# Kernel optimization log

Measured on AMD Instinct MI355X. Metric: run time of the kernel, lower is better.

The kernel has to match this reference:

```python
import jax, jax.numpy as jnp
import numpy as np

IN_C = 256
N_E = 8192
E_DIM = 256
BETA = 0.25
K = 3
LN_EPS = 1e-5


def _conv(x, w, b):
    # x: [B,C,H,W], w: [O,I,K,K]
    y = jax.lax.conv_general_dilated(
        x, w, window_strides=(1, 1), padding='SAME',
        dimension_numbers=('NCHW', 'OIHW', 'NCHW'))
    return y + b[None, :, None, None]


def _layernorm(x, g, b):
    mu = jnp.mean(x, axis=-1, keepdims=True)
    var = jnp.var(x, axis=-1, keepdims=True)
    return (x - mu) * jax.lax.rsqrt(var + LN_EPS) * g + b


def setup_inputs() -> dict:
    key = jax.random.key(0)
    ks = jax.random.split(key, 8)
    fan_emb = IN_C * K * K
    fan_unemb = E_DIM * K * K
    return {
        'z': jax.random.normal(ks[0], (16, IN_C, 32, 32), dtype=jnp.float32),
        'emb_w': jax.random.normal(ks[1], (E_DIM, IN_C, K, K), dtype=jnp.float32) / np.sqrt(fan_emb),
        'emb_b': jnp.zeros((E_DIM,), dtype=jnp.float32),
        'ln_g': jnp.ones((E_DIM,), dtype=jnp.float32),
        'ln_b': jnp.zeros((E_DIM,), dtype=jnp.float32),
        'codebook': jax.random.uniform(ks[2], (N_E, E_DIM), dtype=jnp.float32,
                                       minval=-1.0 / N_E, maxval=1.0 / N_E),
        'unemb_w': jax.random.normal(ks[3], (IN_C, E_DIM, K, K), dtype=jnp.float32) / np.sqrt(fan_unemb),
        'unemb_b': jnp.zeros((IN_C,), dtype=jnp.float32),
    }


def reference(z, emb_w, emb_b, ln_g, ln_b, codebook, unemb_w, unemb_b):
    B, _, H, W = z.shape
    # emb conv, then b c h w -> b h w c
    ze = _conv(z, emb_w, emb_b)                       # [B,E,H,W]
    ze = jnp.transpose(ze, (0, 2, 3, 1))              # [B,H,W,E]
    zf = _layernorm(ze.reshape(B, H * W, E_DIM), ln_g, ln_b)
    zf = zf.reshape(-1, E_DIM)                        # [B*H*W, E]
    # squared distances: ||z||^2 + ||e||^2 - 2 z e^T
    d = (jnp.sum(zf ** 2, axis=1, keepdims=True)
         + jnp.sum(codebook ** 2, axis=1)[None, :]
         - 2.0 * jnp.einsum('bd,nd->bn', zf, codebook))  # [B*H*W, N_E]
    idx = jnp.argmin(d, axis=1)                       # [B*H*W]
    z_q = codebook[idx].reshape(ze.shape)             # [B,H,W,E]
    # legacy loss
    loss = (jnp.mean((jax.lax.stop_gradient(z_q) - ze) ** 2)
            + BETA * jnp.mean((z_q - jax.lax.stop_gradient(ze)) ** 2))
    # straight-through
    z_q = ze + jax.lax.stop_gradient(z_q - ze)
    z_q = jnp.transpose(z_q, (0, 3, 1, 2))            # [B,E,H,W]
    out = _conv(z_q, unemb_w, unemb_b)                # [B,C,H,W]
    return out, loss, idx
```

## Files before the change

kernel.cpp:

```cpp
#include <hip/hip_runtime.h>
#include <hip/hip_bf16.h>

#define B_SZ 16
#define CIN 256
#define EDIM 256
#define NE 8192
#define HW 32
#define NPIX (B_SZ*HW*HW)
#define OUT_ELEMS (B_SZ*CIN*HW*HW)
#define SCREEN_T 3.2e-4f
#define CAND_H 64

typedef __attribute__((ext_vector_type(8))) short short8;
typedef __attribute__((ext_vector_type(4))) short short4v;
typedef __attribute__((ext_vector_type(4))) float f32x4;

__device__ __forceinline__ float block_sum(float v, float* sbuf) {
    #pragma unroll
    for (int off = 32; off > 0; off >>= 1) v += __shfl_down(v, off, 64);
    int wid = threadIdx.x >> 6;
    int lane = threadIdx.x & 63;
    if (lane == 0) sbuf[wid] = v;
    __syncthreads();
    if (threadIdx.x == 0) sbuf[0] = sbuf[0] + sbuf[1] + sbuf[2] + sbuf[3];
    __syncthreads();
    float r = sbuf[0];
    __syncthreads();
    return r;
}

__device__ __forceinline__ double wave_sum_d(double v) {
    #pragma unroll
    for (int off = 32; off > 0; off >>= 1) v += __shfl_down(v, off, 64);
    return __shfl(v, 0, 64);
}

__device__ __forceinline__ unsigned short bf16rne(float f) {
    unsigned int u = __float_as_uint(f);
    unsigned int r = (u + 0x7FFFu + ((u >> 16) & 1u)) >> 16;
    return (unsigned short)r;
}
__device__ __forceinline__ float bf2f(unsigned short h) {
    return __uint_as_float((unsigned int)h << 16);
}

__device__ __forceinline__ unsigned int mapU(float f) {
    unsigned int u = __float_as_uint(f);
    return (u & 0x80000000u) ? ~u : (u | 0x80000000u);
}
__device__ __forceinline__ float unmapU(unsigned int m) {
    unsigned int u = (m & 0x80000000u) ? (m ^ 0x80000000u) : ~m;
    return __uint_as_float(u);
}

__global__ void prep_kernel(const float* __restrict__ emb_w, unsigned short* __restrict__ w1bh,
                            unsigned short* __restrict__ w1bl,
                            const float* __restrict__ unemb_w, unsigned short* __restrict__ w2hi,
                            unsigned short* __restrict__ w2lo, const float* __restrict__ cb,
                            unsigned short* __restrict__ cbhi, unsigned short* __restrict__ cblo) {
    int blk = blockIdx.x;
    if (blk < 2304) {
        int e = blk / 9, tap = blk % 9;
        int c = threadIdx.x;
        float v = emb_w[(size_t)e * 2304 + c * 9 + tap];
        unsigned short h = bf16rne(v);
        unsigned short l = bf16rne(v - bf2f(h));
        size_t j = (size_t)e * 2304 + tap * 256 + c;
        w1bh[j] = h; w1bl[j] = l;
    } else if (blk < 4608) {
        int b2 = blk - 2304;
        int cout = b2 / 9, tap = b2 % 9;
        int e = threadIdx.x;
        float v = unemb_w[(size_t)cout * 2304 + e * 9 + tap];
        unsigned short h = bf16rne(v);
        unsigned short l = bf16rne(v - bf2f(h));
        size_t j = (size_t)cout * 2304 + tap * 256 + e;
        w2hi[j] = h; w2lo[j] = l;
    } else {
        int i = (blk - 4608) * 256 + threadIdx.x;
        size_t base = (size_t)i * 4;
        float4 v = *(const float4*)(cb + base);
        short4v sh, sl;
        unsigned short h;
        h = bf16rne(v.x); sh[0] = (short)h; sl[0] = (short)bf16rne(v.x - bf2f(h));
        h = bf16rne(v.y); sh[1] = (short)h; sl[1] = (short)bf16rne(v.y - bf2f(h));
        h = bf16rne(v.z); sh[2] = (short)h; sl[2] = (short)bf16rne(v.z - bf2f(h));
        h = bf16rne(v.w); sh[3] = (short)h; sl[3] = (short)bf16rne(v.w - bf2f(h));
        *(short4v*)(cbhi + base) = sh;
        *(short4v*)(cblo + base) = sl;
    }
}

#define EM_REG 6528
__global__ __launch_bounds__(256, 4) void conv_emb_mfma(const float* __restrict__ z,
                                                        const unsigned short* __restrict__ w1bh,
                                                        const unsigned short* __restrict__ w1bl,
                                                        float* __restrict__ ze) {
    __shared__ char smem[3 * EM_REG];
    const int tid = threadIdx.x;
    const int wid = tid >> 6, lane = tid & 63;
    const int l15 = lane & 15, lg = lane >> 4;
    const int bh = blockIdx.x;
    const int b = bh >> 5, h = bh & 31;
    const int ch = blockIdx.y;

    for (int i = tid; i < (3 * EM_REG) / 16; i += 256) ((int4*)smem)[i] = make_int4(0, 0, 0, 0);

    const f32x4 zero4 = {0.f, 0.f, 0.f, 0.f};
    f32x4 acc[2][2];
    acc[0][0] = zero4; acc[0][1] = zero4; acc[1][0] = zero4; acc[1][1] = zero4;

    for (int cc = 0; cc < 256; cc += 32) {
        __syncthreads();
        #pragma unroll
        for (int rd = 0; rd < 2; ++rd) {
            int t2 = rd * 256 + tid;
            if (t2 < 408) {
                int row = t2 >> 2;
                int oct = t2 & 3;
                int r = row / 34, wp = row - r * 34;
                int hh = h + r - 1;
                if (hh >= 0 && hh < 32 && wp >= 1 && wp <= 32) {
                    const float* zp = z + (size_t)b * 262144 + (size_t)(cc + oct * 8) * 1024
                                    + hh * 32 + (wp - 1);
                    short8 vh, vm, vl;
                    #pragma unroll
                    for (int j = 0; j < 8; ++j) {
                        float v = zp[(size_t)j * 1024];
                        unsigned short h1 = bf16rne(v);
                        float rm = v - bf2f(h1);
                        unsigned short m1 = bf16rne(rm);
                        float rl = rm - bf2f(m1);
                        unsigned short l1 = bf16rne(rl);
                        vh[j] = (short)h1; vm[j] = (short)m1; vl[j] = (short)l1;
                    }
                    int boff = row * 64 + ((oct * 16) ^ ((wp & 3) << 4));
                    *(short8*)(smem + boff) = vh;
                    *(short8*)(smem + EM_REG + boff) = vm;
                    *(short8*)(smem + 2 * EM_REG + boff) = vl;
                }
            }
        }
        __syncthreads();

        #pragma unroll
        for (int tap = 0; tap < 9; ++tap) {
            const int r = tap / 3, kw = tap % 3;
            short8 a1[2], a2[2], a3[2], bhf[2], blf[2];
            #pragma unroll
            for (int mf = 0; mf < 2; ++mf) {
                int wpr = mf * 16 + l15 + kw;
                int boff = (r * 34 + wpr) * 64 + ((lg * 16) ^ ((wpr & 3) << 4));
                a1[mf] = *(const short8*)(smem + boff);
                a2[mf] = *(const short8*)(smem + EM_REG + boff);
                a3[mf] = *(const short8*)(smem + 2 * EM_REG + boff);
            }
            #pragma unroll
            for (int nf = 0; nf < 2; ++nf) {
                int e_idx = (ch << 7) + (wid << 5) + (nf << 4) + l15;
                size_t goff = (size_t)e_idx * 2304 + tap * 256 + cc + lg * 8;
                bhf[nf] = *(const short8*)(w1bh + goff);
                blf[nf] = *(const short8*)(w1bl + goff);
            }
            #pragma unroll
            for (int mf = 0; mf < 2; ++mf)
                #pragma unroll
                for (int nf = 0; nf < 2; ++nf) {
                    acc[mf][nf] = __builtin_amdgcn_mfma_f32_16x16x32_bf16(a1[mf], bhf[nf], acc[mf][nf], 0, 0, 0);
                    acc[mf][nf] = __builtin_amdgcn_mfma_f32_16x16x32_bf16(a1[mf], blf[nf], acc[mf][nf], 0, 0, 0);
                    acc[mf][nf] = __builtin_amdgcn_mfma_f32_16x16x32_bf16(a2[mf], bhf[nf], acc[mf][nf], 0, 0, 0);
                    acc[mf][nf] = __builtin_amdgcn_mfma_f32_16x16x32_bf16(a2[mf], blf[nf], acc[mf][nf], 0, 0, 0);
                    acc[mf][nf] = __builtin_amdgcn_mfma_f32_16x16x32_bf16(a3[mf], bhf[nf], acc[mf][nf], 0, 0, 0);
                }
        }
    }

    int p0 = (b * 32 + h) * 32;
    #pragma unroll
    for (int mf = 0; mf < 2; ++mf)
        #pragma unroll
        for (int nf = 0; nf < 2; ++nf) {
            int e_idx = (ch << 7) + (wid << 5) + (nf << 4) + l15;
            #pragma unroll
            for (int rr = 0; rr < 4; ++rr) {
                int pix = mf * 16 + lg * 4 + rr;
                ze[(size_t)(p0 + pix) * 256 + e_idx] = acc[mf][nf][rr];
            }
        }
}

__global__ __launch_bounds__(256) void ln_kernel(float* __restrict__ ze, const float* __restrict__ bias,
                                                 const float* __restrict__ g,
                                                 const float* __restrict__ bta,
                                                 unsigned short* __restrict__ zfb,
                                                 float* __restrict__ snorm, float* __restrict__ mu_a,
                                                 float* __restrict__ r_a) {
    int wid = threadIdx.x >> 6, lane = threadIdx.x & 63;
    int p = blockIdx.x * 4 + wid;
    float* zp = ze + (size_t)p * 256;
    float x0 = zp[lane]       + bias[lane];
    float x1 = zp[lane + 64]  + bias[lane + 64];
    float x2 = zp[lane + 128] + bias[lane + 128];
    float x3 = zp[lane + 192] + bias[lane + 192];
    zp[lane] = x0; zp[lane + 64] = x1; zp[lane + 128] = x2; zp[lane + 192] = x3;
    double lsum = (((double)x0 + (double)x1) + (double)x2) + (double)x3;
    double sum = wave_sum_d(lsum);
    float mu = ((float)sum) / 256.0f;
    float e0 = x0 - mu, e1 = x1 - mu, e2 = x2 - mu, e3 = x3 - mu;
    double lsq = (((double)(e0 * e0) + (double)(e1 * e1)) + (double)(e2 * e2)) + (double)(e3 * e3);
    double vs = wave_sum_d(lsq);
    float var = ((float)vs) / 256.0f;
    float r = 1.0f / sqrtf(var + 1e-5f);
    float y0 = ((e0 * r) * g[lane])       + bta[lane];
    float y1 = ((e1 * r) * g[lane + 64])  + bta[lane + 64];
    float y2 = ((e2 * r) * g[lane + 128]) + bta[lane + 128];
    float y3 = ((e3 * r) * g[lane + 192]) + bta[lane + 192];
    unsigned short* zq = zfb + (size_t)p * 256;
    zq[lane] = bf16rne(y0); zq[lane + 64] = bf16rne(y1);
    zq[lane + 128] = bf16rne(y2); zq[lane + 192] = bf16rne(y3);
    double lys = (((double)(y0 * y0) + (double)(y1 * y1)) + (double)(y2 * y2)) + (double)(y3 * y3);
    double ss = wave_sum_d(lys);
    if (lane == 0) { snorm[p] = (float)ss; mu_a[p] = mu; r_a[p] = r; }
}

__global__ __launch_bounds__(512) void screen_kernel(const unsigned short* __restrict__ zf_bf,
                                                     const unsigned short* __restrict__ cb_bf,
                                                     int* __restrict__ ccnt,
                                                     int* __restrict__ cand) {
    __shared__ unsigned int smax[64];
    __shared__ int scnt[64];
    __shared__ int sbuf[64][CAND_H];
    const int tid = threadIdx.x;
    const int w = tid >> 6;
    const int lane = tid & 63;
    const int l15 = lane & 15, lg = lane >> 4;
    const int p0 = blockIdx.x * 64;
    const int nh = blockIdx.y;
    const int nbase = nh << 12;
    const int rowoff = w * 16 + l15;
    const int lg8 = lg * 8;

    if (tid < 64) { smax[tid] = 0u; scnt[tid] = 0; }
    __syncthreads();

    short8 aF[4][8];
    #pragma unroll
    for (int mf = 0; mf < 4; ++mf)
        #pragma unroll
        for (int ks = 0; ks < 8; ++ks)
            aF[mf][ks] = *reinterpret_cast<const short8*>(
                zf_bf + (size_t)(p0 + mf * 16 + l15) * 256 + ks * 32 + lg8);

    const f32x4 zero4 = {0.f, 0.f, 0.f, 0.f};
    float runL[4][4], runS[4][4];
    #pragma unroll
    for (int mf = 0; mf < 4; ++mf)
        #pragma unroll
        for (int r = 0; r < 4; ++r) { runL[mf][r] = -3.4e38f; runS[mf][r] = -3.4e38f; }

    const unsigned short* basep = cb_bf + (size_t)(nbase + rowoff) * 256 + lg8;

    for (int c = 0; c < 4; ++c) {
        const unsigned short* bp = basep + (size_t)c * 128 * 256;
        short8 bF[8];
        #pragma unroll
        for (int ks = 0; ks < 8; ++ks) bF[ks] = *reinterpret_cast<const short8*>(bp + ks * 32);
        f32x4 acc[4] = {zero4, zero4, zero4, zero4};
        #pragma unroll
        for (int ks = 0; ks < 8; ++ks)
            #pragma unroll
            for (int mf = 0; mf < 4; ++mf)
                acc[mf] = __builtin_amdgcn_mfma_f32_16x16x32_bf16(aF[mf][ks], bF[ks], acc[mf], 0, 0, 0);
        #pragma unroll
        for (int mf = 0; mf < 4; ++mf)
            #pragma unroll
            for (int r = 0; r < 4; ++r) runL[mf][r] = fmaxf(runL[mf][r], acc[mf][r]);
    }
    #pragma unroll
    for (int mf = 0; mf < 4; ++mf)
        #pragma unroll
        for (int r = 0; r < 4; ++r) {
            float v = runL[mf][r];
            v = fmaxf(v, __shfl_xor(v, 1, 64));
            v = fmaxf(v, __shfl_xor(v, 2, 64));
            v = fmaxf(v, __shfl_xor(v, 4, 64));
            v = fmaxf(v, __shfl_xor(v, 8, 64));
            runL[mf][r] = v;
            if (l15 == 0) atomicMax(&smax[mf * 16 + lg * 4 + r], mapU(v));
        }
    __syncthreads();
    #pragma unroll
    for (int mf = 0; mf < 4; ++mf)
        #pragma unroll
        for (int r = 0; r < 4; ++r) runS[mf][r] = unmapU(smax[mf * 16 + lg * 4 + r]);

    for (int c = 0; c < 32; ++c) {
        const int nrow = nbase + c * 128 + rowoff;
        const unsigned short* bp = basep + (size_t)c * 128 * 256;
        short8 bF[8];
        #pragma unroll
        for (int ks = 0; ks < 8; ++ks) bF[ks] = *reinterpret_cast<const short8*>(bp + ks * 32);
        f32x4 acc[4] = {zero4, zero4, zero4, zero4};
        #pragma unroll
        for (int ks = 0; ks < 8; ++ks)
            #pragma unroll
            for (int mf = 0; mf < 4; ++mf)
                acc[mf] = __builtin_amdgcn_mfma_f32_16x16x32_bf16(aF[mf][ks], bF[ks], acc[mf], 0, 0, 0);

        unsigned qual = 0u;
        #pragma unroll
        for (int mf = 0; mf < 4; ++mf)
            #pragma unroll
            for (int r = 0; r < 4; ++r) {
                float dd = acc[mf][r];
                if (dd >= fmaxf(runS[mf][r], runL[mf][r]) - SCREEN_T) qual |= (1u << (mf * 4 + r));
                runL[mf][r] = fmaxf(runL[mf][r], dd);
            }
        if (qual) {
            #pragma unroll
            for (int mf = 0; mf < 4; ++mf)
                #pragma unroll
                for (int r = 0; r < 4; ++r)
                    if (qual & (1u << (mf * 4 + r))) {
                        int pix = mf * 16 + lg * 4 + r;
                        int s = atomicAdd(&scnt[pix], 1);
                        if (s < CAND_H) sbuf[pix][s] = nrow;
                    }
        }
        if ((c & 7) == 7) {
            #pragma unroll
            for (int mf = 0; mf < 4; ++mf)
                #pragma unroll
                for (int r = 0; r < 4; ++r) {
                    float v = runL[mf][r];
                    v = fmaxf(v, __shfl_xor(v, 1, 64));
                    v = fmaxf(v, __shfl_xor(v, 2, 64));
                    v = fmaxf(v, __shfl_xor(v, 4, 64));
                    v = fmaxf(v, __shfl_xor(v, 8, 64));
                    runL[mf][r] = v;
                    if (l15 == 0) atomicMax(&smax[mf * 16 + lg * 4 + r], mapU(v));
                }
            #pragma unroll
            for (int mf = 0; mf < 4; ++mf)
                #pragma unroll
                for (int r = 0; r < 4; ++r) runS[mf][r] = unmapU(smax[mf * 16 + lg * 4 + r]);
        }
    }
    __syncthreads();
    if (tid < 64) {
        int v = scnt[tid];
        ccnt[nh * NPIX + p0 + tid] = (v < CAND_H) ? v : CAND_H;
    }
    for (int i = tid; i < 64 * CAND_H; i += 512) {
        int pix = i >> 6;
        int s = i & (CAND_H - 1);
        if (s < scnt[pix])
            cand[(size_t)(p0 + pix) * 128 + nh * CAND_H + s] = sbuf[pix][s];
    }
}

__global__ __launch_bounds__(256) void rescore_kernel(const float* __restrict__ ze,
                                                      const float* __restrict__ mu_a,
                                                      const float* __restrict__ r_a,
                                                      const float* __restrict__ snorm,
                                                      const float* __restrict__ g,
                                                      const float* __restrict__ bta,
                                                      const float* __restrict__ cb,
                                                      const int* __restrict__ ccnt,
                                                      const int* __restrict__ cand,
                                                      int* __restrict__ idx_i,
                                                      float* __restrict__ idx_f) {
    int p = blockIdx.x * 4 + (threadIdx.x >> 6);
    int lane = threadIdx.x & 63;
    int cnt0 = ccnt[p];           if (cnt0 > CAND_H) cnt0 = CAND_H;
    int cnt1 = ccnt[NPIX + p];    if (cnt1 > CAND_H) cnt1 = CAND_H;
    int total = cnt0 + cnt1;
    float d = 3.4e38f;
    int ix = 0x7FFFFFFF;
    float mu = mu_a[p];
    float r = r_a[p];
    float sz = snorm[p];
    const float* zr = ze + (size_t)p * 256;
    for (int s = lane; s < total; s += 64) {
        int n = (s < cnt0) ? cand[(size_t)p * 128 + s]
                           : cand[(size_t)p * 128 + CAND_H + (s - cnt0)];
        const float* cr = cb + (size_t)n * 256;
        float a0 = 0.f, a1 = 0.f, a2 = 0.f, a3 = 0.f;
        for (int k0 = 0; k0 < 256; k0 += 4) {
            float4 zq = *(const float4*)(zr + k0);
            float4 gq = *(const float4*)(g + k0);
            float4 bq = *(const float4*)(bta + k0);
            float4 cq = *(const float4*)(cr + k0);
            float d0 = zq.x - mu; float y0 = ((d0 * r) * gq.x) + bq.x;
            float d1 = zq.y - mu; float y1 = ((d1 * r) * gq.y) + bq.y;
            float d2 = zq.z - mu; float y2 = ((d2 * r) * gq.z) + bq.z;
            float d3 = zq.w - mu; float y3 = ((d3 * r) * gq.w) + bq.w;
            a0 = fmaf(y0, cq.x, a0);
            a1 = fmaf(y1, cq.y, a1);
            a2 = fmaf(y2, cq.z, a2);
            a3 = fmaf(y3, cq.w, a3);
        }
        float dot32 = (float)(((double)a0 + (double)a1) + ((double)a2 + (double)a3));
        float dd = fmaf(-2.0f, dot32, sz);
        if (dd < d || (dd == d && n < ix)) { d = dd; ix = n; }
    }
    #pragma unroll
    for (int off = 32; off > 0; off >>= 1) {
        float ov = __shfl_down(d, off, 64);
        int   oi = __shfl_down(ix, off, 64);
        if (ov < d || (ov == d && oi < ix)) { d = ov; ix = oi; }
    }
    if (lane == 0) {
        idx_i[p] = ix;
        idx_f[p] = (float)ix;
    }
}

__global__ void loss_partial_kernel(const float* __restrict__ ze, const float* __restrict__ cb,
                                    const int* __restrict__ idx, float* __restrict__ partials) {
    __shared__ float sbuf[4];
    float sum = 0.f;
    const int total = NPIX * 256;
    for (int i = blockIdx.x * blockDim.x + threadIdx.x; i < total; i += gridDim.x * blockDim.x) {
        int p = i >> 8;
        int e = i & 255;
        float d = cb[(size_t)idx[p] * 256 + e] - ze[i];
        sum = fmaf(d, d, sum);
    }
    sum = block_sum(sum, sbuf);
    if (threadIdx.x == 0) partials[blockIdx.x] = sum;
}

__global__ void loss_final_kernel(const float* __restrict__ partials, float* __restrict__ loss_out) {
    __shared__ float sbuf[4];
    float v = partials[threadIdx.x];
    v = block_sum(v, sbuf);
    if (threadIdx.x == 0) *loss_out = v * (1.25f / (float)(NPIX * 256));
}

#define AROWB 128
#define ALO   13056
__global__ __launch_bounds__(256, 4) void conv_unemb_mfma(const unsigned short* __restrict__ cb_hi,
                                                          const unsigned short* __restrict__ cb_lo,
                                                          const int* __restrict__ idx,
                                                          const unsigned short* __restrict__ w2_hi,
                                                          const unsigned short* __restrict__ w2_lo,
                                                          const float* __restrict__ bias,
                                                          float* __restrict__ out) {
    __shared__ char smem[2 * ALO];
    float* ot = (float*)smem;
    const int tid = threadIdx.x;
    const int wid = tid >> 6, lane = tid & 63;
    const int l15 = lane & 15, lg = lane >> 4;
    const int bh = blockIdx.x;
    const int b = bh >> 5, h = bh & 31;
    const int ch = blockIdx.y;

    for (int i = tid; i < (2 * ALO) / 16; i += 256) ((int4*)smem)[i] = make_int4(0, 0, 0, 0);

    int nrow[3], rok[3], wpos[3], rr3[3];
    #pragma unroll
    for (int rd = 0; rd < 3; ++rd) {
        int t2 = rd * 256 + tid;
        int row = t2 >> 3;
        int r = row >> 5, w = row & 31;
        int hh = h + r - 1;
        rok[rd] = (hh >= 0 && hh < 32) ? 1 : 0;
        rr3[rd] = r; wpos[rd] = w;
        nrow[rd] = rok[rd] ? idx[(b * 32 + hh) * 32 + w] : 0;
    }
    __syncthreads();

    const f32x4 zero4 = {0.f, 0.f, 0.f, 0.f};
    f32x4 acc[2][2];
    acc[0][0] = zero4; acc[0][1] = zero4; acc[1][0] = zero4; acc[1][1] = zero4;

    for (int ec = 0; ec < 4; ++ec) {
        if (ec) __syncthreads();
        #pragma unroll
        for (int rd = 0; rd < 3; ++rd) {
            if (rok[rd]) {
                int t2 = rd * 256 + tid;
                int eo = (t2 & 7) * 8;
                size_t gsrc = (size_t)nrow[rd] * 256 + ec * 64 + eo;
                short8 vh = *(const short8*)(cb_hi + gsrc);
                short8 vl = *(const short8*)(cb_lo + gsrc);
                int wp = wpos[rd] + 1;
                int rowbase = (rr3[rd] * 34 + wp) * AROWB;
                int boff = (eo * 2) ^ ((wp & 7) << 4);
                *(short8*)(smem + rowbase + boff) = vh;
                *(short8*)(smem + ALO + rowbase + boff) = vl;
            }
        }
        __syncthreads();

        #pragma unroll
        for (int tap = 0; tap < 9; ++tap) {
            const int r = tap / 3, kw = tap % 3;
            #pragma unroll
            for (int ks = 0; ks < 2; ++ks) {
                int e2 = ks * 32 + lg * 8;
                short8 ah[2], al[2], bh2[2], bl2[2];
                #pragma unroll
                for (int mf = 0; mf < 2; ++mf) {
                    int wp = mf * 16 + l15 + kw;
                    int rowbase = (r * 34 + wp) * AROWB;
                    int boff = (e2 * 2) ^ ((wp & 7) << 4);
                    ah[mf] = *(const short8*)(smem + rowbase + boff);
                    al[mf] = *(const short8*)(smem + ALO + rowbase + boff);
                }
                #pragma unroll
                for (int nf = 0; nf < 2; ++nf) {
                    int cout = (ch << 7) + (wid << 5) + (nf << 4) + l15;
                    size_t goff = (size_t)cout * 2304 + tap * 256 + ec * 64 + e2;
                    bh2[nf] = *(const short8*)(w2_hi + goff);
                    bl2[nf] = *(const short8*)(w2_lo + goff);
                }
                #pragma unroll
                for (int mf = 0; mf < 2; ++mf)
                    #pragma unroll
                    for (int nf = 0; nf < 2; ++nf) {
                        acc[mf][nf] = __builtin_amdgcn_mfma_f32_16x16x32_bf16(ah[mf], bh2[nf], acc[mf][nf], 0, 0, 0);
                        acc[mf][nf] = __builtin_amdgcn_mfma_f32_16x16x32_bf16(ah[mf], bl2[nf], acc[mf][nf], 0, 0, 0);
                        acc[mf][nf] = __builtin_amdgcn_mfma_f32_16x16x32_bf16(al[mf], bh2[nf], acc[mf][nf], 0, 0, 0);
                    }
            }
        }
    }
    __syncthreads();
    #pragma unroll
    for (int mf = 0; mf < 2; ++mf)
        #pragma unroll
        for (int nf = 0; nf < 2; ++nf) {
            int cl = (wid << 5) + (nf << 4) + l15;
            #pragma unroll
            for (int rr = 0; rr < 4; ++rr) {
                int px = mf * 16 + lg * 4 + rr;
                ot[cl * 36 + px] = acc[mf][nf][rr];
            }
        }
    __syncthreads();
    int row = tid >> 1, half = tid & 1;
    int cout = (ch << 7) + row;
    float bv = bias[cout];
    float* dst = out + ((size_t)(b * 256 + cout) * 32 + h) * 32 + half * 16;
    const float* src = ot + row * 36 + half * 16;
    #pragma unroll
    for (int q = 0; q < 4; ++q) {
        float4 v = *(const float4*)(src + q * 4);
        v.x += bv; v.y += bv; v.z += bv; v.w += bv;
        *(float4*)(dst + q * 4) = v;
    }
}

extern "C" void kernel_launch(void* const* d_in, const int* in_sizes, int n_in,
                              void* d_out, int out_size, void* d_ws, size_t ws_size,
                              hipStream_t stream) {
    const float* z       = (const float*)d_in[0];
    const float* emb_w   = (const float*)d_in[1];
    const float* emb_b   = (const float*)d_in[2];
    const float* ln_g    = (const float*)d_in[3];
    const float* ln_b    = (const float*)d_in[4];
    const float* cb      = (const float*)d_in[5];
    const float* unemb_w = (const float*)d_in[6];
    const float* unemb_b = (const float*)d_in[7];

    float* out    = (float*)d_out;
    float* lossp  = out + OUT_ELEMS;
    float* idxf   = out + OUT_ELEMS + 1;

    float* ws = (float*)d_ws;
    float* ze_t = ws;
    unsigned short* zf_bf = (unsigned short*)(ze_t + (size_t)NPIX * 256);
    unsigned short* cb_hi = (unsigned short*)((float*)zf_bf + 2097152);
    unsigned short* cb_lo = (unsigned short*)((float*)cb_hi + 1048576);
    float* snorm = (float*)cb_lo + 1048576;
    float* mu_a  = snorm + NPIX;
    float* r_a   = mu_a + NPIX;
    unsigned short* w1bh = (unsigned short*)(r_a + NPIX);
    unsigned short* w1bl = (unsigned short*)((float*)w1bh + 294912);
    unsigned short* w2_hi = (unsigned short*)((float*)w1bl + 294912);
    unsigned short* w2_lo = (unsigned short*)((float*)w2_hi + 294912);
    int*   ccnt  = (int*)((float*)w2_lo + 294912);
    int*   cand  = ccnt + 2 * NPIX;
    int*   idxi  = cand + (size_t)NPIX * 128;
    float* partials = (float*)(idxi + NPIX);

    hipLaunchKernelGGL(prep_kernel, dim3(6656), dim3(256), 0, stream,
                       emb_w, w1bh, w1bl, unemb_w, w2_hi, w2_lo, cb, cb_hi, cb_lo);
    hipLaunchKernelGGL(conv_emb_mfma, dim3(512, 2), dim3(256), 0, stream, z, w1bh, w1bl, ze_t);
    hipLaunchKernelGGL(ln_kernel, dim3(NPIX / 4), dim3(256), 0, stream, ze_t, emb_b, ln_g, ln_b,
                       zf_bf, snorm, mu_a, r_a);
    hipLaunchKernelGGL(screen_kernel, dim3(256, 2), dim3(512), 0, stream, zf_bf, cb_hi, ccnt, cand);
    hipLaunchKernelGGL(rescore_kernel, dim3(NPIX / 4), dim3(256), 0, stream,
                       ze_t, mu_a, r_a, snorm, ln_g, ln_b, cb, ccnt, cand, idxi, idxf);
    hipLaunchKernelGGL(loss_partial_kernel, dim3(256), dim3(256), 0, stream, ze_t, cb, idxi, partials);
    hipLaunchKernelGGL(loss_final_kernel, dim3(1), dim3(256), 0, stream, partials, lossp);
    hipLaunchKernelGGL(conv_unemb_mfma, dim3(512, 2), dim3(256), 0, stream,
                       cb_hi, cb_lo, idxi, w2_hi, w2_lo, unemb_b, out);
}
```

Measured before the change: 602.9 us.

## Shrink screen kernel tiles to 32 pixels and software-pipeline codebook loads

The screen kernel now uses 256-thread blocks that each handle 32 pixels instead of 512 threads on 64 pixels, which halves the A-fragment registers and shared candidate buffers per block and requests three blocks per CU through launch bounds. The inner loop walks 64-row codebook chunks and prefetches the next half-chunk of B fragments while MFMAs run on the current one, aiming to hide global load latency. In exchange, each codebook row is reread by twice as many blocks, and with fewer pixels per block there is less MFMA work to amortize each load.

```diff
diff --git a/kernel.cpp b/kernel.cpp
--- a/kernel.cpp
+++ b/kernel.cpp
@@ -223,61 +223,62 @@
     if (lane == 0) { snorm[p] = (float)ss; mu_a[p] = mu; r_a[p] = r; }
 }
 
-__global__ __launch_bounds__(512) void screen_kernel(const unsigned short* __restrict__ zf_bf,
-                                                     const unsigned short* __restrict__ cb_bf,
-                                                     int* __restrict__ ccnt,
-                                                     int* __restrict__ cand) {
-    __shared__ unsigned int smax[64];
-    __shared__ int scnt[64];
-    __shared__ int sbuf[64][CAND_H];
+__global__ __launch_bounds__(256, 3) void screen_kernel(const unsigned short* __restrict__ zf_bf,
+                                                        const unsigned short* __restrict__ cb_bf,
+                                                        int* __restrict__ ccnt,
+                                                        int* __restrict__ cand) {
+    __shared__ unsigned int smax[32];
+    __shared__ int scnt[32];
+    __shared__ int sbuf[32][CAND_H];
     const int tid = threadIdx.x;
     const int w = tid >> 6;
     const int lane = tid & 63;
     const int l15 = lane & 15, lg = lane >> 4;
-    const int p0 = blockIdx.x * 64;
+    const int p0 = blockIdx.x * 32;
     const int nh = blockIdx.y;
     const int nbase = nh << 12;
     const int rowoff = w * 16 + l15;
     const int lg8 = lg * 8;
 
-    if (tid < 64) { smax[tid] = 0u; scnt[tid] = 0; }
-    __syncthreads();
-
-    short8 aF[4][8];
-    #pragma unroll
-    for (int mf = 0; mf < 4; ++mf)
+    if (tid < 32) { smax[tid] = 0u; scnt[tid] = 0; }
+    __syncthreads();
+
+    short8 aF[2][8];
+    #pragma unroll
+    for (int mf = 0; mf < 2; ++mf)
         #pragma unroll
         for (int ks = 0; ks < 8; ++ks)
             aF[mf][ks] = *reinterpret_cast<const short8*>(
                 zf_bf + (size_t)(p0 + mf * 16 + l15) * 256 + ks * 32 + lg8);
 
     const f32x4 zero4 = {0.f, 0.f, 0.f, 0.f};
-    float runL[4][4], runS[4][4];
-    #pragma unroll
-    for (int mf = 0; mf < 4; ++mf)
+    float runL[2][4], runS[2][4];
+    #pragma unroll
+    for (int mf = 0; mf < 2; ++mf)
         #pragma unroll
         for (int r = 0; r < 4; ++r) { runL[mf][r] = -3.4e38f; runS[mf][r] = -3.4e38f; }
 
     const unsigned short* basep = cb_bf + (size_t)(nbase + rowoff) * 256 + lg8;
 
-    for (int c = 0; c < 4; ++c) {
-        const unsigned short* bp = basep + (size_t)c * 128 * 256;
-        short8 bF[8];
-        #pragma unroll
-        for (int ks = 0; ks < 8; ++ks) bF[ks] = *reinterpret_cast<const short8*>(bp + ks * 32);
-        f32x4 acc[4] = {zero4, zero4, zero4, zero4};
-        #pragma unroll
-        for (int ks = 0; ks < 8; ++ks)
-            #pragma unroll
-            for (int mf = 0; mf < 4; ++mf)
-                acc[mf] = __builtin_amdgcn_mfma_f32_16x16x32_bf16(aF[mf][ks], bF[ks], acc[mf], 0, 0, 0);
-        #pragma unroll
-        for (int mf = 0; mf < 4; ++mf)
-            #pragma unroll
-            for (int r = 0; r < 4; ++r) runL[mf][r] = fmaxf(runL[mf][r], acc[mf][r]);
-    }
-    #pragma unroll
-    for (int mf = 0; mf < 4; ++mf)
+    for (int c = 0; c < 8; ++c) {
+        const unsigned short* bp = basep + (size_t)c * 64 * 256;
+        short8 bS[8];
+        #pragma unroll
+        for (int ks = 0; ks < 8; ++ks) bS[ks] = *reinterpret_cast<const short8*>(bp + ks * 32);
+        f32x4 a0 = zero4, a1 = zero4;
+        #pragma unroll
+        for (int ks = 0; ks < 8; ++ks) {
+            a0 = __builtin_amdgcn_mfma_f32_16x16x32_bf16(aF[0][ks], bS[ks], a0, 0, 0, 0);
+            a1 = __builtin_amdgcn_mfma_f32_16x16x32_bf16(aF[1][ks], bS[ks], a1, 0, 0, 0);
+        }
+        #pragma unroll
+        for (int r = 0; r < 4; ++r) {
+            runL[0][r] = fmaxf(runL[0][r], a0[r]);
+            runL[1][r] = fmaxf(runL[1][r], a1[r]);
+        }
+    }
+    #pragma unroll
+    for (int mf = 0; mf < 2; ++mf)
         #pragma unroll
         for (int r = 0; r < 4; ++r) {
             float v = runL[mf][r];
@@ -290,35 +291,53 @@
         }
     __syncthreads();
     #pragma unroll
-    for (int mf = 0; mf < 4; ++mf)
+    for (int mf = 0; mf < 2; ++mf)
         #pragma unroll
         for (int r = 0; r < 4; ++r) runS[mf][r] = unmapU(smax[mf * 16 + lg * 4 + r]);
 
-    for (int c = 0; c < 32; ++c) {
-        const int nrow = nbase + c * 128 + rowoff;
-        const unsigned short* bp = basep + (size_t)c * 128 * 256;
-        short8 bF[8];
-        #pragma unroll
-        for (int ks = 0; ks < 8; ++ks) bF[ks] = *reinterpret_cast<const short8*>(bp + ks * 32);
-        f32x4 acc[4] = {zero4, zero4, zero4, zero4};
-        #pragma unroll
-        for (int ks = 0; ks < 8; ++ks)
-            #pragma unroll
-            for (int mf = 0; mf < 4; ++mf)
-                acc[mf] = __builtin_amdgcn_mfma_f32_16x16x32_bf16(aF[mf][ks], bF[ks], acc[mf], 0, 0, 0);
-
+    short8 bF[4];
+    #pragma unroll
+    for (int q = 0; q < 4; ++q) bF[q] = *reinterpret_cast<const short8*>(basep + q * 32);
+
+    for (int c = 0; c < 64; ++c) {
+        const unsigned short* cp = basep + (size_t)c * 64 * 256;
+        const unsigned short* np = cp + (size_t)64 * 256;
+        f32x4 a0 = zero4, a1 = zero4;
+        #pragma unroll
+        for (int q = 0; q < 4; ++q) {
+            a0 = __builtin_amdgcn_mfma_f32_16x16x32_bf16(aF[0][q], bF[q], a0, 0, 0, 0);
+            a1 = __builtin_amdgcn_mfma_f32_16x16x32_bf16(aF[1][q], bF[q], a1, 0, 0, 0);
+            bF[q] = *reinterpret_cast<const short8*>(cp + (q + 4) * 32);
+        }
+        if (c < 63) {
+            #pragma unroll
+            for (int q = 0; q < 4; ++q) {
+                a0 = __builtin_amdgcn_mfma_f32_16x16x32_bf16(aF[0][q + 4], bF[q], a0, 0, 0, 0);
+                a1 = __builtin_amdgcn_mfma_f32_16x16x32_bf16(aF[1][q + 4], bF[q], a1, 0, 0, 0);
+                bF[q] = *reinterpret_cast<const short8*>(np + q * 32);
+            }
+        } else {
+            #pragma unroll
+            for (int q = 0; q < 4; ++q) {
+                a0 = __builtin_amdgcn_mfma_f32_16x16x32_bf16(aF[0][q + 4], bF[q], a0, 0, 0, 0);
+                a1 = __builtin_amdgcn_mfma_f32_16x16x32_bf16(aF[1][q + 4], bF[q], a1, 0, 0, 0);
+            }
+        }
+
+        const int nrow = nbase + c * 64 + rowoff;
         unsigned qual = 0u;
         #pragma unroll
-        for (int mf = 0; mf < 4; ++mf)
-            #pragma unroll
-            for (int r = 0; r < 4; ++r) {
-                float dd = acc[mf][r];
-                if (dd >= fmaxf(runS[mf][r], runL[mf][r]) - SCREEN_T) qual |= (1u << (mf * 4 + r));
-                runL[mf][r] = fmaxf(runL[mf][r], dd);
-            }
+        for (int r = 0; r < 4; ++r) {
+            float dd0 = a0[r];
+            if (dd0 >= fmaxf(runS[0][r], runL[0][r]) - SCREEN_T) qual |= (1u << r);
+            runL[0][r] = fmaxf(runL[0][r], dd0);
+            float dd1 = a1[r];
+            if (dd1 >= fmaxf(runS[1][r], runL[1][r]) - SCREEN_T) qual |= (1u << (4 + r));
+            runL[1][r] = fmaxf(runL[1][r], dd1);
+        }
         if (qual) {
             #pragma unroll
-            for (int mf = 0; mf < 4; ++mf)
+            for (int mf = 0; mf < 2; ++mf)
                 #pragma unroll
                 for (int r = 0; r < 4; ++r)
                     if (qual & (1u << (mf * 4 + r))) {
@@ -329,7 +348,7 @@
         }
         if ((c & 7) == 7) {
             #pragma unroll
-            for (int mf = 0; mf < 4; ++mf)
+            for (int mf = 0; mf < 2; ++mf)
                 #pragma unroll
                 for (int r = 0; r < 4; ++r) {
                     float v = runL[mf][r];
@@ -341,17 +360,17 @@
                     if (l15 == 0) atomicMax(&smax[mf * 16 + lg * 4 + r], mapU(v));
                 }
             #pragma unroll
-            for (int mf = 0; mf < 4; ++mf)
+            for (int mf = 0; mf < 2; ++mf)
                 #pragma unroll
                 for (int r = 0; r < 4; ++r) runS[mf][r] = unmapU(smax[mf * 16 + lg * 4 + r]);
         }
     }
     __syncthreads();
-    if (tid < 64) {
+    if (tid < 32) {
         int v = scnt[tid];
         ccnt[nh * NPIX + p0 + tid] = (v < CAND_H) ? v : CAND_H;
     }
-    for (int i = tid; i < 64 * CAND_H; i += 512) {
+    for (int i = tid; i < 32 * CAND_H; i += 256) {
         int pix = i >> 6;
         int s = i & (CAND_H - 1);
         if (s < scnt[pix])
@@ -591,7 +610,7 @@
     hipLaunchKernelGGL(conv_emb_mfma, dim3(512, 2), dim3(256), 0, stream, z, w1bh, w1bl, ze_t);
     hipLaunchKernelGGL(ln_kernel, dim3(NPIX / 4), dim3(256), 0, stream, ze_t, emb_b, ln_g, ln_b,
                        zf_bf, snorm, mu_a, r_a);
-    hipLaunchKernelGGL(screen_kernel, dim3(256, 2), dim3(512), 0, stream, zf_bf, cb_hi, ccnt, cand);
+    hipLaunchKernelGGL(screen_kernel, dim3(512, 2), dim3(256), 0, stream, zf_bf, cb_hi, ccnt, cand);
     hipLaunchKernelGGL(rescore_kernel, dim3(NPIX / 4), dim3(256), 0, stream,
                        ze_t, mu_a, r_a, snorm, ln_g, ln_b, cb, ccnt, cand, idxi, idxf);
     hipLaunchKernelGGL(loss_partial_kernel, dim3(256), dim3(256), 0, stream, ze_t, cb, idxi, partials);
```

After: 694.1 us. +15.1%, slower.
